# Optimization experiments

Hardware: AMD Instinct MI355X
Metric: run time of the kernel (lower is better)

The kernel has to match this reference:

```python
import jax, jax.numpy as jnp
import numpy as np

N, E, D, ED, B, MAXN, GF, MIX = 1024, 2048, 256, 128, 16, 64, 38, 10
EPS = 1e-5


def setup_inputs() -> dict:
    key = jax.random.key(0)
    ks = jax.random.split(key, 16)

    def w(k, shape, fan_in, scale=1.0):
        return jax.random.normal(k, shape, jnp.float32) * (scale / np.sqrt(fan_in))

    return {
        "x": jax.random.normal(ks[0], (N, GF), jnp.float32),
        "edge_attr": jax.random.uniform(ks[1], (E, 4), jnp.float32),
        "edge_index": jax.random.randint(ks[2], (2, E), 0, N),
        "lin_w": w(ks[3], (D, GF), GF), "lin_b": jnp.zeros((D,), jnp.float32),
        "bn_g": jnp.ones((D,), jnp.float32), "bn_b": jnp.zeros((D,), jnp.float32),
        "nn_w1": w(ks[4], (ED, 4), 4), "nn_b1": jnp.zeros((ED,), jnp.float32),
        "nn_w2": w(ks[5], (D * D, ED), ED, 0.1), "nn_b2": jnp.zeros((D * D,), jnp.float32),
        "root_w": w(ks[6], (D, D), D), "conv_b": jnp.zeros((D,), jnp.float32),
        "gru_wih": w(ks[7], (3 * D, D), D), "gru_whh": w(ks[8], (3 * D, D), D),
        "gru_bih": jnp.zeros((3 * D,), jnp.float32), "gru_bhh": jnp.zeros((3 * D,), jnp.float32),
        "mlp_w1": w(ks[9], (MIX, D, D), D), "mlp_b1": jnp.zeros((MIX, D), jnp.float32),
        "mlp_w2": w(ks[10], (MIX, D, D), D), "mlp_b2": jnp.zeros((MIX, D), jnp.float32),
        "mlp_w3": w(ks[11], (MIX, 1, D), D), "mlp_b3": jnp.zeros((MIX, 1), jnp.float32),
    }


def reference(x, edge_attr, edge_index, lin_w, lin_b, bn_g, bn_b, nn_w1, nn_b1,
              nn_w2, nn_b2, root_w, conv_b, gru_wih, gru_whh, gru_bih, gru_bhh,
              mlp_w1, mlp_b1, mlp_w2, mlp_b2, mlp_w3, mlp_b3):
    src, dst = edge_index[0], edge_index[1]

    # input embed + BatchNorm1d (training-mode batch statistics)
    y = x @ lin_w.T + lin_b
    mean, var = y.mean(0), y.var(0)
    xh = (y - mean) / jnp.sqrt(var + EPS) * bn_g + bn_b

    # edge-conditioned NNConv weights: per-edge [D, D] matrix from edge MLP
    hidden = jax.nn.sigmoid(edge_attr @ nn_w1.T + nn_b1)          # [E, ED]
    We = (hidden @ nn_w2.T + nn_b2).reshape(E, D, D)               # [E, D, D]

    cnt = jax.ops.segment_sum(jnp.ones((E,), jnp.float32), dst, num_segments=N)
    denom = jnp.maximum(cnt, 1.0)[:, None]                         # mean aggregation

    def conv(xn):
        msg = jnp.einsum('ed,edf->ef', xn[src], We)                # per-edge matmul
        agg = jax.ops.segment_sum(msg, dst, num_segments=N) / denom
        return agg + xn @ root_w.T + conv_b                        # NNConv root + bias

    def gru(xn, h):                                                # torch GRU cell math
        gi = xn @ gru_wih.T + gru_bih
        gh = h @ gru_whh.T + gru_bhh
        ir, iz, inn = jnp.split(gi, 3, -1)
        hr, hz, hn = jnp.split(gh, 3, -1)
        r = jax.nn.sigmoid(ir + hr)
        z = jax.nn.sigmoid(iz + hz)
        n = jnp.tanh(inn + r * hn)
        return (1.0 - z) * n + z * h

    h = xh
    xc = xh
    for _ in range(3):
        m = jax.nn.relu(conv(xc))
        h = gru(m, h)
        xc = h

    vert = xc.reshape(B, MAXN, D)                                  # [B, MAX_N, D]
    h1 = jax.nn.relu(jnp.einsum('bnd,mkd->mbnk', vert, mlp_w1) + mlp_b1[:, None, None, :])
    h2 = jax.nn.relu(jnp.einsum('mbnk,mjk->mbnj', h1, mlp_w2) + mlp_b2[:, None, None, :])
    mix = jnp.einsum('mbnk,mjk->mbnj', h2, mlp_w3) + mlp_b3[:, None, None, :]  # [MIX,B,MAX_N,1]

    # bootstrap_compute, eval mode: mean over mixtures, unbiased std
    mu = mix.mean(0)
    std = jnp.sqrt(mix.var(0, ddof=1) + EPS)
    return mu, std
```

## Files before the change

### kernel.cpp

```cpp
#include <hip/hip_runtime.h>
#include <hip/hip_bf16.h>
#include <math.h>

typedef _Float16 f16;
typedef _Float16 f16x8 __attribute__((ext_vector_type(8)));
typedef _Float16 f16x4 __attribute__((ext_vector_type(4)));
typedef _Float16 f16x2 __attribute__((ext_vector_type(2)));
typedef _Float16 half2v __attribute__((ext_vector_type(2)));
typedef float    f32x4 __attribute__((ext_vector_type(4)));

#define NN 1024
#define EE 2048
#define DD 256
#define EDH 128

typedef const __attribute__((address_space(1))) void gas_t;
typedef __attribute__((address_space(3))) void las_t;
#define GLOAD16(g, l) __builtin_amdgcn_global_load_lds((gas_t*)(g), (las_t*)(l), 16, 0, 0)

#if __has_builtin(__builtin_amdgcn_fdot2)
#define DOT2(a, b, c) __builtin_amdgcn_fdot2((a), (b), (c), false)
#else
#define DOT2(a, b, c) ((float)(a)[0]*(float)(b)[0] + (float)(a)[1]*(float)(b)[1] + (c))
#endif


__global__ __launch_bounds__(256) void k_embed_hidden(const float* __restrict__ x,
    const float* __restrict__ lw, const float* __restrict__ lb,
    const float* __restrict__ ea, const float* __restrict__ w1, const float* __restrict__ b1,
    float* __restrict__ y, float* __restrict__ colsum, float* __restrict__ colsq,
    f16* __restrict__ h16e) {
  int bid = blockIdx.x, t = threadIdx.x;
  if (bid < 256) {
    int n0 = bid*4;
    __shared__ float xr[4][38];
    if (t < 152) ((float*)xr)[t] = x[n0*38 + t];
    __syncthreads();
    float b0 = lb[t];
    float s0 = b0, s1 = b0, s2 = b0, s3 = b0;
    const float* w = lw + t*38;
    #pragma unroll
    for (int d = 0; d < 38; d++) {
      float wd = w[d];
      s0 += xr[0][d]*wd; s1 += xr[1][d]*wd; s2 += xr[2][d]*wd; s3 += xr[3][d]*wd;
    }
    y[(n0+0)*DD + t] = s0; y[(n0+1)*DD + t] = s1;
    y[(n0+2)*DD + t] = s2; y[(n0+3)*DD + t] = s3;
    atomicAdd(&colsum[t], s0+s1+s2+s3);
    atomicAdd(&colsq[t], s0*s0+s1*s1+s2*s2+s3*s3);
  } else {
    int e = (bid - 256)*2 + (t >> 7);
    int k = t & 127;
    const float* a = ea + e*4;
    const float* w = w1 + k*4;
    float s = b1[k] + a[0]*w[0] + a[1]*w[1] + a[2]*w[2] + a[3]*w[3];
    h16e[e*EDH + k] = (f16)(1.f / (1.f + expf(-s)));
  }
}

__global__ __launch_bounds__(256) void k_bnapply(const float* __restrict__ y,
    const float* __restrict__ colsum, const float* __restrict__ colsq,
    const float* __restrict__ g, const float* __restrict__ b,
    float* __restrict__ xh, f16* __restrict__ xc16) {
  int i = blockIdx.x*256 + threadIdx.x;
  int c = i & 255;
  float mean = colsum[c] * (1.f/1024.f);
  float var  = colsq[c] * (1.f/1024.f) - mean*mean;
  float sc = g[c] / sqrtf(var + 1e-5f);
  float sh = b[c] - mean*sc;
  float v = y[i]*sc + sh;
  xh[i] = v;
  xc16[i] = (f16)v;
}


__global__ __launch_bounds__(1024) void k_csr(const int* __restrict__ ei,
    int* __restrict__ cntAll, int* __restrict__ offAll, float* __restrict__ denomB,
    unsigned* __restrict__ rec, int* __restrict__ srcD) {
  __shared__ int cntD[1024], cntS[1024], curD[1024], curS[1024], sc[1024];
  int t = threadIdx.x;
  cntD[t] = 0; cntS[t] = 0;
  __syncthreads();
  #pragma unroll
  for (int r = 0; r < 2; r++) {
    int e = r*1024 + t;
    atomicAdd(&cntD[ei[EE + e]], 1);
    atomicAdd(&cntS[ei[e]], 1);
  }
  __syncthreads();
  int cD = cntD[t], cS = cntS[t];
  sc[t] = cD; __syncthreads();
  for (int o = 1; o < 1024; o <<= 1) {
    int v = (t >= o) ? sc[t - o] : 0;
    __syncthreads(); sc[t] += v; __syncthreads();
  }
  int exD = sc[t] - cD;
  curD[t] = exD;
  cntAll[t] = cD; offAll[t] = exD;
  denomB[t] = (float)(cD > 1 ? cD : 1);
  __syncthreads();
  sc[t] = cS; __syncthreads();
  for (int o = 1; o < 1024; o <<= 1) {
    int v = (t >= o) ? sc[t - o] : 0;
    __syncthreads(); sc[t] += v; __syncthreads();
  }
  int exS = sc[t] - cS;
  curS[t] = exS;
  offAll[1024 + t] = exS;
  __syncthreads();
  #pragma unroll
  for (int r = 0; r < 2; r++) {
    int e = r*1024 + t;
    int d = ei[EE + e], s2 = ei[e];
    int pD = atomicAdd(&curD[d], 1);
    int pS = atomicAdd(&curS[s2], 1);
    rec[pS] = (unsigned)e | ((unsigned)s2 << 11) | ((unsigned)pD << 21);
    srcD[pD] = s2;
  }
}


__global__ __launch_bounds__(256) void k_w2tr(const float* __restrict__ w2, f16* __restrict__ BTb) {
  __shared__ f16 ls[128][130];
  int f = blockIdx.x, dh = blockIdx.y, t = threadIdx.x;
  int dl = t >> 1, kh = (t & 1) * 64;
  const float* src = w2 + ((size_t)(dh*128 + dl)*256 + f)*128 + kh;
  #pragma unroll
  for (int i = 0; i < 16; i++) {
    f32x4 v = *(const f32x4*)(src + i*4);
    f16x2 a = {(f16)v[0], (f16)v[1]};
    f16x2 b = {(f16)v[2], (f16)v[3]};
    *(f16x2*)(&ls[dl][kh + i*4])     = a;
    *(f16x2*)(&ls[dl][kh + i*4 + 2]) = b;
  }
  __syncthreads();
  int k = t >> 1, dh2 = (t & 1) * 64;
  f16* dst = BTb + ((size_t)f*128 + k)*256 + dh*128 + dh2;
  #pragma unroll
  for (int g = 0; g < 8; g++) {
    f16x8 pk;
    #pragma unroll
    for (int q = 0; q < 8; q++) pk[q] = ls[dh2 + g*8 + q][k];
    *(f16x8*)(dst + g*8) = pk;
  }
}


__global__ __launch_bounds__(256) void k_prepw(const float* __restrict__ s0, f16* __restrict__ d0,
    const float* __restrict__ s1, f16* __restrict__ d1,
    const float* __restrict__ s2, f16* __restrict__ d2,
    const float* __restrict__ s3, f16* __restrict__ d3,
    const float* __restrict__ rw, const float* __restrict__ nb2, f16* __restrict__ Bside) {
  int bid = blockIdx.x, t = threadIdx.x;
  if (bid < 1664) {
    const float* src; f16* dst; int i;
    if      (bid < 192)  { src = s0; dst = d0; i = bid*256 + t; }
    else if (bid < 384)  { src = s1; dst = d1; i = (bid-192)*256 + t; }
    else if (bid < 1024) { src = s2; dst = d2; i = (bid-384)*256 + t; }
    else                 { src = s3; dst = d3; i = (bid-1024)*256 + t; }
    f32x4 v = ((const f32x4*)src)[i];
    f16x4 r; r[0]=(f16)v[0]; r[1]=(f16)v[1]; r[2]=(f16)v[2]; r[3]=(f16)v[3];
    ((f16x4*)dst)[i] = r;
  } else if (bid < 1728) {
    int i = (bid - 1664)*256 + t;
    f32x4 v = *(const f32x4*)(rw + (size_t)i*4);
    f16x4 r; r[0]=(f16)v[0]; r[1]=(f16)v[1]; r[2]=(f16)v[2]; r[3]=(f16)v[3];
    *(f16x4*)(Bside + 65536 + (size_t)i*4) = r;
  } else {
    __shared__ float ls[64][65];
    int fb = bid - 1728;
    for (int db = 0; db < 4; db++) {
      int r = t >> 2, cs = (t & 3) * 16;
      const float* s = nb2 + (size_t)(db*64 + r)*256 + fb*64 + cs;
      #pragma unroll
      for (int i = 0; i < 16; i += 4) {
        f32x4 v = *(const f32x4*)(s + i);
        ls[r][cs+i] = v[0]; ls[r][cs+i+1] = v[1]; ls[r][cs+i+2] = v[2]; ls[r][cs+i+3] = v[3];
      }
      __syncthreads();
      int fl = t >> 2, ds2 = (t & 3) * 16;
      f16x8 p0, p1;
      #pragma unroll
      for (int q = 0; q < 8; q++) { p0[q] = (f16)ls[ds2+q][fl]; p1[q] = (f16)ls[ds2+8+q][fl]; }
      f16* d = Bside + (size_t)(fb*64 + fl)*256 + db*64 + ds2;
      *(f16x8*)(d)     = p0;
      *(f16x8*)(d + 8) = p1;
      __syncthreads();
    }
  }
}


__global__ __launch_bounds__(256) void k_fgemm(const f16* __restrict__ A,
    const f16* __restrict__ BTb, const f16* __restrict__ Bside, const f16* __restrict__ Wbh,
    const f16* __restrict__ h16e, const int* __restrict__ offAll,
    const unsigned* __restrict__ rec, float* __restrict__ T2R,
    float* __restrict__ G2, float* __restrict__ msgbuf) {
  __shared__ __align__(16) f16 lds[12288];
  int raw = blockIdx.x;
  int pmod = raw & 7, q = raw >> 3;
  int m = q & 15, pg = q >> 4;
  int p = pg*8 + pmod;
  if (p >= 266) return;
  int m0 = m*64;
  int t = threadIdx.x;
  int lane = t & 63, wv = t >> 6, wm = wv >> 1, wn = wv & 1;
  int lr = lane & 15, lg = lane >> 4;
  const f16* Bbase = (p < 256) ? (BTb + (size_t)p*32768)
                   : (p < 260) ? (Bside + (size_t)(p-256)*32768)
                               : (Wbh + (size_t)(p-260)*32768);
  int ea = wv*512 + lane*8;
  int ra = ea >> 5, ca = ea & 31;
  const f16* AgA = A + (size_t)(m0 + ra)*256 + ca;
  int e0 = wv*1024 + lane*8;
  int r0 = e0 >> 5, c0 = e0 & 31;
  int e1 = e0 + 512;
  int r1 = e1 >> 5, c1 = e1 & 31;
  const f16* Bg0 = Bbase + (size_t)r0*256 + c0;
  const f16* Bg1 = Bbase + (size_t)r1*256 + c1;
  f16* As = lds;
  f16* Bs = lds + 4096;
  f16* AlA = As + wv*512;
  f16* Bl0 = Bs + wv*1024; f16* Bl1 = Bl0 + 512;
  f32x4 acc[2][4] = {};
  for (int k0 = 0; k0 < 256; k0 += 64) {
    __syncthreads();
    GLOAD16(AgA + k0,      AlA);
    GLOAD16(AgA + k0 + 32, AlA + 2048);
    GLOAD16(Bg0 + k0,      Bl0);
    GLOAD16(Bg1 + k0,      Bl1);
    GLOAD16(Bg0 + k0 + 32, Bl0 + 4096);
    GLOAD16(Bg1 + k0 + 32, Bl1 + 4096);
    __syncthreads();
    #pragma unroll
    for (int P = 0; P < 2; P++) {
      f16x8 af[2], bf[4];
      #pragma unroll
      for (int i = 0; i < 2; i++)
        af[i] = *(const f16x8*)(&As[P*2048 + (wm*32 + i*16 + lr)*32 + lg*8]);
      #pragma unroll
      for (int j = 0; j < 4; j++)
        bf[j] = *(const f16x8*)(&Bs[P*4096 + (wn*64 + j*16 + lr)*32 + lg*8]);
      #pragma unroll
      for (int i = 0; i < 2; i++)
        #pragma unroll
        for (int j = 0; j < 4; j++)
          acc[i][j] = __builtin_amdgcn_mfma_f32_16x16x32_f16(af[i], bf[j], acc[i][j], 0, 0, 0);
    }
  }
  if (p >= 260) {
    int c0o = (p - 260)*128;
    #pragma unroll
    for (int i = 0; i < 2; i++)
      #pragma unroll
      for (int j = 0; j < 4; j++)
        #pragma unroll
        for (int v = 0; v < 4; v++)
          G2[(size_t)(m0 + wm*32 + i*16 + lg*4 + v)*768 + c0o + wn*64 + j*16 + lr] = acc[i][j][v];
    return;
  }
  if (p >= 256) {
    int c0o = (p - 256)*128;
    #pragma unroll
    for (int i = 0; i < 2; i++)
      #pragma unroll
      for (int j = 0; j < 4; j++)
        #pragma unroll
        for (int v = 0; v < 4; v++)
          T2R[(size_t)(m0 + wm*32 + i*16 + lg*4 + v)*512 + c0o + wn*64 + j*16 + lr] = acc[i][j][v];
    return;
  }
  __syncthreads();
  #pragma unroll
  for (int i = 0; i < 2; i++)
    #pragma unroll
    for (int j = 0; j < 4; j++)
      #pragma unroll
      for (int v = 0; v < 4; v++) {
        int r = wm*32 + i*16 + lg*4 + v;
        int c = wn*64 + j*16 + lr;
        lds[r*128 + (((c >> 3) ^ (r & 7)) << 3) + (c & 7)] = (f16)acc[i][j][v];
      }
  __syncthreads();
  int eS = offAll[1024 + m0];
  int eE = (m0 + 64 < 1024) ? offAll[1024 + m0 + 64] : EE;
  int g = t & 1, es = t >> 1;
  for (int idx = eS + es; idx < eE; idx += 128) {
    unsigned u = rec[idx];
    int e = u & 2047, src = (u >> 11) & 1023, pos = (int)(u >> 21);
    int r = src - m0;
    const f16* hp = h16e + (size_t)e*EDH + g*64;
    float s0 = 0.f, s1 = 0.f;
    #pragma unroll
    for (int i = 0; i < 8; i++) {
      int blk = g*8 + i;
      f16x8 hv = *(const f16x8*)(hp + i*8);
      f16x8 tv = *(const f16x8*)(&lds[r*128 + ((blk ^ (r & 7)) << 3)]);
      union { f16x8 v8; half2v pr[4]; } hu, tu;
      hu.v8 = hv; tu.v8 = tv;
      float sx = (i & 1) ? s1 : s0;
      #pragma unroll
      for (int qd = 0; qd < 4; qd++) sx = DOT2(hu.pr[qd], tu.pr[qd], sx);
      if (i & 1) s1 = sx; else s0 = sx;
    }
    float s = s0 + s1;
    s += __shfl_xor(s, 1, 64);
    if (g == 0) msgbuf[(size_t)pos*256 + p] = s;
  }
}


__global__ __launch_bounds__(256) void k_fin(const float* __restrict__ msgbuf,
    const int* __restrict__ cntAll, const int* __restrict__ offAll,
    const float* __restrict__ denomB, const float* __restrict__ T2R,
    const int* __restrict__ srcD, const float* __restrict__ cb, f16* __restrict__ Am) {
  int n = blockIdx.x, t = threadIdx.x;
  int deg = cntAll[n], o = offAll[n];
  float s = 0.f;
  for (int j = 0; j < deg; j++)
    s += msgbuf[(size_t)(o+j)*256 + t] + T2R[(size_t)srcD[o+j]*512 + t];
  float m = s / denomB[n] + T2R[(size_t)n*512 + 256 + t] + cb[t];
  Am[(size_t)n*256 + t] = (f16)fmaxf(m, 0.f);
}


__global__ __launch_bounds__(256) void k_gemm64(const f16* __restrict__ A,
    const f16* __restrict__ BT, float* __restrict__ C) {
  __shared__ __align__(16) f16 As[64*40];
  __shared__ __align__(16) f16 Bs[64*40];
  int t = threadIdx.x;
  int m0 = blockIdx.x*64, n0 = blockIdx.y*64;
  int lane = t & 63, wv = t >> 6, wm = wv >> 1, wn = wv & 1;
  int lr = lane & 15, lk = (lane >> 4) * 8;
  int arow = t >> 2, aseg = (t & 3) * 8;
  f32x4 acc[2][2] = {};
  for (int k0 = 0; k0 < 256; k0 += 32) {
    __syncthreads();
    *(f16x8*)(&As[arow*40 + aseg]) = *(const f16x8*)(A + (size_t)(m0 + arow)*256 + k0 + aseg);
    *(f16x8*)(&Bs[arow*40 + aseg]) = *(const f16x8*)(BT + (size_t)(n0 + arow)*256 + k0 + aseg);
    __syncthreads();
    f16x8 af[2], bf[2];
    #pragma unroll
    for (int i = 0; i < 2; i++) af[i] = *(const f16x8*)(&As[(wm*32 + i*16 + lr)*40 + lk]);
    #pragma unroll
    for (int j = 0; j < 2; j++) bf[j] = *(const f16x8*)(&Bs[(wn*32 + j*16 + lr)*40 + lk]);
    #pragma unroll
    for (int i = 0; i < 2; i++)
      #pragma unroll
      for (int j = 0; j < 2; j++)
        acc[i][j] = __builtin_amdgcn_mfma_f32_16x16x32_f16(af[i], bf[j], acc[i][j], 0, 0, 0);
  }
  #pragma unroll
  for (int i = 0; i < 2; i++)
    #pragma unroll
    for (int j = 0; j < 2; j++)
      #pragma unroll
      for (int v = 0; v < 4; v++) {
        int r = m0 + wm*32 + i*16 + (lane >> 4)*4 + v;
        int cc = n0 + wn*32 + j*16 + lr;
        C[(size_t)r*768 + cc] = acc[i][j][v];
      }
}


template<int MODE>
__global__ __launch_bounds__(256) void k_gemm_sm(const f16* __restrict__ A,
    const f16* __restrict__ BT, float* __restrict__ C, f16* __restrict__ Ch,
    const float* __restrict__ bias, int K, int lda, int ldb, int N,
    int bsA, int bsB, int bsC, int bsBias) {
  __shared__ __align__(16) f16 As[64*40];
  __shared__ __align__(16) f16 Bs[128*40];
  int t = threadIdx.x;
  int m0 = blockIdx.x*64, n0 = blockIdx.y*128, z = blockIdx.z;
  A  += (size_t)z * bsA;
  BT += (size_t)z * bsB;
  if constexpr (MODE == 1) C += (size_t)z * bsC;
  else { Ch += (size_t)z * bsC; bias += (size_t)z * bsBias; }
  int lane = t & 63, wv = t >> 6, wm = wv >> 1, wn = wv & 1;
  int lr = lane & 15, lk = (lane >> 4) * 8;
  int arow = t >> 2, aseg = (t & 3) * 8;
  f32x4 acc[2][4] = {};
  for (int k0 = 0; k0 < K; k0 += 32) {
    __syncthreads();
    *(f16x8*)(&As[arow*40 + aseg]) = *(const f16x8*)(A + (size_t)(m0 + arow)*lda + k0 + aseg);
    *(f16x8*)(&Bs[arow*40 + aseg]) = *(const f16x8*)(BT + (size_t)(n0 + arow)*ldb + k0 + aseg);
    *(f16x8*)(&Bs[(64+arow)*40 + aseg]) = *(const f16x8*)(BT + (size_t)(n0 + 64 + arow)*ldb + k0 + aseg);
    __syncthreads();
    f16x8 af[2], bf[4];
    #pragma unroll
    for (int i = 0; i < 2; i++) af[i] = *(const f16x8*)(&As[(wm*32 + i*16 + lr)*40 + lk]);
    #pragma unroll
    for (int j = 0; j < 4; j++) bf[j] = *(const f16x8*)(&Bs[(wn*64 + j*16 + lr)*40 + lk]);
    #pragma unroll
    for (int i = 0; i < 2; i++)
      #pragma unroll
      for (int j = 0; j < 4; j++)
        acc[i][j] = __builtin_amdgcn_mfma_f32_16x16x32_f16(af[i], bf[j], acc[i][j], 0, 0, 0);
  }
  #pragma unroll
  for (int i = 0; i < 2; i++)
    #pragma unroll
    for (int j = 0; j < 4; j++)
      #pragma unroll
      for (int v = 0; v < 4; v++) {
        int r = m0 + wm*32 + i*16 + (lane >> 4)*4 + v;
        int cc = n0 + wn*64 + j*16 + lr;
        float val = acc[i][j][v];
        if constexpr (MODE == 1) {
          C[(size_t)r*N + cc] = val;
        } else {
          val += bias[cc];
          val = fmaxf(val, 0.f);
          Ch[(size_t)r*N + cc] = (f16)val;
        }
      }
}


__global__ __launch_bounds__(256) void k_gate(const float* __restrict__ gi,
    const float* __restrict__ gh, const float* __restrict__ bih, const float* __restrict__ bhh,
    const float* __restrict__ hOld, float* __restrict__ hNew, f16* __restrict__ xc16) {
  int i = blockIdx.x*256 + threadIdx.x;
  int row = i >> 8, c = i & 255;
  const float* gir = gi + (size_t)row*768;
  const float* ghr = gh + (size_t)row*768;
  float ir  = gir[c]     + bih[c],     hr = ghr[c]     + bhh[c];
  float iz  = gir[256+c] + bih[256+c], hz = ghr[256+c] + bhh[256+c];
  float inn = gir[512+c] + bih[512+c], hn = ghr[512+c] + bhh[512+c];
  float r  = 1.f / (1.f + expf(-(ir + hr)));
  float zz = 1.f / (1.f + expf(-(iz + hz)));
  float nn = tanhf(inn + r*hn);
  float hv = (1.f - zz)*nn + zz*hOld[i];
  hNew[i] = hv;
  xc16[i] = (f16)hv;
}


__global__ __launch_bounds__(256) void k_mix(const f16* __restrict__ h2,
    const float* __restrict__ w3, const float* __restrict__ b3, float* __restrict__ mix) {
  int b = blockIdx.x, t = threadIdx.x;
  int wv = t >> 6, lane = t & 63;
  int rid = b*4 + wv;
  int m = rid >> 10, row = rid & 1023;
  const f16* hr = h2 + (size_t)(m*1024 + row)*DD;
  const float* w = w3 + m*DD;
  float s = 0.f;
  #pragma unroll
  for (int q = 0; q < 4; q++) { int d = lane + q*64; s += (float)hr[d] * w[d]; }
  #pragma unroll
  for (int o = 32; o; o >>= 1) s += __shfl_down(s, o, 64);
  if (lane == 0) mix[m*1024 + row] = s + b3[m];
}

__global__ __launch_bounds__(256) void k_out(const float* __restrict__ mix, float* __restrict__ out) {
  int i = blockIdx.x*256 + threadIdx.x;
  float v[10]; float mu = 0.f;
  #pragma unroll
  for (int m = 0; m < 10; m++) { v[m] = mix[m*1024 + i]; mu += v[m]; }
  mu *= 0.1f;
  float var = 0.f;
  #pragma unroll
  for (int m = 0; m < 10; m++) { float d = v[m] - mu; var += d*d; }
  var *= (1.f/9.f);
  out[i] = mu;
  out[1024 + i] = sqrtf(var + 1e-5f);
}


extern "C" void kernel_launch(void* const* d_in, const int* in_sizes, int n_in,
                              void* d_out, int out_size, void* d_ws, size_t ws_size,
                              hipStream_t stream) {
  const float* x         = (const float*)d_in[0];
  const float* edge_attr = (const float*)d_in[1];
  const int*   edge_idx  = (const int*)  d_in[2];
  const float* lin_w     = (const float*)d_in[3];
  const float* lin_b     = (const float*)d_in[4];
  const float* bn_g      = (const float*)d_in[5];
  const float* bn_b      = (const float*)d_in[6];
  const float* nn_w1     = (const float*)d_in[7];
  const float* nn_b1     = (const float*)d_in[8];
  const float* nn_w2     = (const float*)d_in[9];
  const float* nn_b2     = (const float*)d_in[10];
  const float* root_w    = (const float*)d_in[11];
  const float* conv_b    = (const float*)d_in[12];
  const float* gru_wih   = (const float*)d_in[13];
  const float* gru_whh   = (const float*)d_in[14];
  const float* gru_bih   = (const float*)d_in[15];
  const float* gru_bhh   = (const float*)d_in[16];
  const float* mlp_w1    = (const float*)d_in[17];
  const float* mlp_b1    = (const float*)d_in[18];
  const float* mlp_w2    = (const float*)d_in[19];
  const float* mlp_b2    = (const float*)d_in[20];
  const float* mlp_w3    = (const float*)d_in[21];
  const float* mlp_b3    = (const float*)d_in[22];
  float* out = (float*)d_out;

  char* w = (char*)d_ws;
  size_t o = 0;
  auto nxt = [&](size_t b) -> size_t { size_t r = o; o += (b + 255) & ~(size_t)255; return r; };
  float* y      = (float*)(w + nxt(1048576));
  float* colsum = (float*)(w + nxt(1024));
  float* colsq  = (float*)(w + nxt(1024));
  float* xh     = (float*)(w + nxt(1048576));
  float* h      = (float*)(w + nxt(1048576));
  f16*   xc16   = (f16*)  (w + nxt(524288));
  f16*   h16e   = (f16*)  (w + nxt(524288));
  int*   cntAll = (int*)  (w + nxt(4096));
  int*   offAll = (int*)  (w + nxt(8192));
  float* denomB = (float*)(w + nxt(4096));
  unsigned* rec = (unsigned*)(w + nxt(8192));
  int*   srcD   = (int*)  (w + nxt(8192));
  f16*   BTb    = (f16*)  (w + nxt((size_t)32768*256*2));
  f16*   Bside  = (f16*)  (w + nxt((size_t)512*256*2));
  float* T2R    = (float*)(w + nxt((size_t)1024*512*4));
  float* msgbuf = (float*)(w + nxt((size_t)EE*256*4));
  f16*   Am     = (f16*)  (w + nxt(524288));
  float* G      = (float*)(w + nxt((size_t)2*1024*768*4));
  f16*   Wb     = (f16*)  (w + nxt(786432));
  f16*   w1T    = (f16*)  (w + nxt(1310720));
  f16*   w2T    = (f16*)  (w + nxt(1310720));
  f16*   h1     = (f16*)  (w + nxt(5242880));
  f16*   h2     = (f16*)  (w + nxt(5242880));
  float* mixb   = (float*)(w + nxt(40960));
  if (o > ws_size) return;

  hipMemsetAsync(colsum, 0, 2048, stream);

  k_embed_hidden<<<1280, 256, 0, stream>>>(x, lin_w, lin_b, edge_attr, nn_w1, nn_b1,
                                           y, colsum, colsq, h16e);
  k_bnapply<<<1024, 256, 0, stream>>>(y, colsum, colsq, bn_g, bn_b, xh, xc16);
  k_csr  <<<1, 1024, 0, stream>>>(edge_idx, cntAll, offAll, denomB, rec, srcD);
  k_w2tr <<<dim3(256, 2), 256, 0, stream>>>(nn_w2, BTb);
  k_prepw<<<1732, 256, 0, stream>>>(gru_wih, Wb, gru_whh, Wb + 196608,
                                    mlp_w1, w1T, mlp_w2, w2T, root_w, nn_b2, Bside);

  for (int it = 0; it < 3; it++) {
    const float* hOld = (it == 0) ? xh : h;
    k_fgemm<<<4352, 256, 0, stream>>>(xc16, BTb, Bside, Wb + 196608, h16e, offAll,
                                      rec, T2R, G + 786432, msgbuf);
    k_fin  <<<1024, 256, 0, stream>>>(msgbuf, cntAll, offAll, denomB, T2R, srcD, conv_b, Am);
    k_gemm64<<<dim3(16, 12), 256, 0, stream>>>(Am, Wb, G);
    k_gate<<<1024, 256, 0, stream>>>(G, G + 786432, gru_bih, gru_bhh, hOld, h, xc16);
  }

  k_gemm_sm<3><<<dim3(16, 2, 10), 256, 0, stream>>>(xc16, w1T, nullptr, h1, mlp_b1,
      256, 256, 256, 256, 0, 65536, 262144, 256);
  k_gemm_sm<3><<<dim3(16, 2, 10), 256, 0, stream>>>(h1, w2T, nullptr, h2, mlp_b2,
      256, 256, 256, 256, 262144, 65536, 262144, 256);
  k_mix<<<2560, 256, 0, stream>>>(h2, mlp_w3, mlp_b3, mixb);
  k_out<<<4, 256, 0, stream>>>(mixb, out);
}
```

Baseline: 238.4 us.

## Double-buffer k_fgemm LDS tiles to overlap global loads with MFMA

Rewrites the k_fgemm main loop from four 64-wide K steps, each with a full sync before compute, into eight 32-wide steps. LDS buffers are double-buffered and the next tile is prefetched with global_load_lds before the current one is consumed, using manual vmcnt waits and raw barriers. It also raises wave priority around the MFMA block. The aim is to hide global load latency behind compute, at the cost of twice as many barriers per tile and a dependence on hand-written waitcnt correctness.

```diff
diff --git a/kernel.cpp b/kernel.cpp
--- a/kernel.cpp
+++ b/kernel.cpp
@@ -209,44 +209,53 @@
   const f16* Bbase = (p < 256) ? (BTb + (size_t)p*32768)
                    : (p < 260) ? (Bside + (size_t)(p-256)*32768)
                                : (Wbh + (size_t)(p-260)*32768);
-  int ea = wv*512 + lane*8;
+  int ea = t*8;
   int ra = ea >> 5, ca = ea & 31;
   const f16* AgA = A + (size_t)(m0 + ra)*256 + ca;
-  int e0 = wv*1024 + lane*8;
-  int r0 = e0 >> 5, c0 = e0 & 31;
-  int e1 = e0 + 512;
-  int r1 = e1 >> 5, c1 = e1 & 31;
-  const f16* Bg0 = Bbase + (size_t)r0*256 + c0;
-  const f16* Bg1 = Bbase + (size_t)r1*256 + c1;
-  f16* As = lds;
-  f16* Bs = lds + 4096;
-  f16* AlA = As + wv*512;
-  f16* Bl0 = Bs + wv*1024; f16* Bl1 = Bl0 + 512;
+  int eb0 = wv*1024 + lane*8;
+  int rb0 = eb0 >> 5, cb0 = eb0 & 31;
+  int eb1 = eb0 + 512;
+  int rb1 = eb1 >> 5, cb1 = eb1 & 31;
+  const f16* Bg0 = Bbase + (size_t)rb0*256 + cb0;
+  const f16* Bg1 = Bbase + (size_t)rb1*256 + cb1;
+  f16* As0 = lds;         f16* As1 = lds + 2048;
+  f16* Bs0 = lds + 4096;  f16* Bs1 = lds + 8192;
+  GLOAD16(AgA, As0 + wv*512);
+  GLOAD16(Bg0, Bs0 + wv*1024);
+  GLOAD16(Bg1, Bs0 + wv*1024 + 512);
   f32x4 acc[2][4] = {};
-  for (int k0 = 0; k0 < 256; k0 += 64) {
-    __syncthreads();
-    GLOAD16(AgA + k0,      AlA);
-    GLOAD16(AgA + k0 + 32, AlA + 2048);
-    GLOAD16(Bg0 + k0,      Bl0);
-    GLOAD16(Bg1 + k0,      Bl1);
-    GLOAD16(Bg0 + k0 + 32, Bl0 + 4096);
-    GLOAD16(Bg1 + k0 + 32, Bl1 + 4096);
-    __syncthreads();
-    #pragma unroll
-    for (int P = 0; P < 2; P++) {
-      f16x8 af[2], bf[4];
-      #pragma unroll
-      for (int i = 0; i < 2; i++)
-        af[i] = *(const f16x8*)(&As[P*2048 + (wm*32 + i*16 + lr)*32 + lg*8]);
+  #pragma unroll
+  for (int k = 0; k < 8; k++) {
+    int cur = k & 1;
+    f16* Ac = cur ? As1 : As0;
+    f16* Bc = cur ? Bs1 : Bs0;
+    if (k < 7) {
+      int k0 = (k + 1) * 32;
+      f16* An = cur ? As0 : As1;
+      f16* Bn = cur ? Bs0 : Bs1;
+      GLOAD16(AgA + k0, An + wv*512);
+      GLOAD16(Bg0 + k0, Bn + wv*1024);
+      GLOAD16(Bg1 + k0, Bn + wv*1024 + 512);
+      asm volatile("s_waitcnt vmcnt(3)" ::: "memory");
+    } else {
+      asm volatile("s_waitcnt vmcnt(0)" ::: "memory");
+    }
+    __builtin_amdgcn_s_barrier();
+    f16x8 af[2], bf[4];
+    #pragma unroll
+    for (int i = 0; i < 2; i++)
+      af[i] = *(const f16x8*)(&Ac[(wm*32 + i*16 + lr)*32 + lg*8]);
+    #pragma unroll
+    for (int j = 0; j < 4; j++)
+      bf[j] = *(const f16x8*)(&Bc[(wn*64 + j*16 + lr)*32 + lg*8]);
+    __builtin_amdgcn_s_setprio(1);
+    #pragma unroll
+    for (int i = 0; i < 2; i++)
       #pragma unroll
       for (int j = 0; j < 4; j++)
-        bf[j] = *(const f16x8*)(&Bs[P*4096 + (wn*64 + j*16 + lr)*32 + lg*8]);
-      #pragma unroll
-      for (int i = 0; i < 2; i++)
-        #pragma unroll
-        for (int j = 0; j < 4; j++)
-          acc[i][j] = __builtin_amdgcn_mfma_f32_16x16x32_f16(af[i], bf[j], acc[i][j], 0, 0, 0);
-    }
+        acc[i][j] = __builtin_amdgcn_mfma_f32_16x16x32_f16(af[i], bf[j], acc[i][j], 0, 0, 0);
+    __builtin_amdgcn_s_setprio(0);
+    __builtin_amdgcn_s_barrier();
   }
   if (p >= 260) {
     int c0o = (p - 260)*128;
@@ -270,7 +279,6 @@
           T2R[(size_t)(m0 + wm*32 + i*16 + lg*4 + v)*512 + c0o + wn*64 + j*16 + lr] = acc[i][j][v];
     return;
   }
-  __syncthreads();
   #pragma unroll
   for (int i = 0; i < 2; i++)
     #pragma unroll
```

After: 241.4 us. No clear change (+1.2%).
